# Kernel optimization log

Measured on AMD Instinct MI355X. Metric: run time of the kernel, lower is better.

Reference implementation:

```python
import jax, jax.numpy as jnp
import numpy as np

B, N, IN_F = 4, 2048, 256
H, HEAD_DIM = 8, 32  # out_features=256, concat=True -> head_dim=32
ALPHA = 0.2
MASK_VAL = -9e15


def setup_inputs() -> dict:
    key = jax.random.key(0)
    k1, k2, k3, k4 = jax.random.split(key, 4)
    x = jax.random.normal(k1, (B, N, IN_F), dtype=jnp.float32)
    adj = jax.random.randint(k2, (B, N, N), 0, 2, dtype=jnp.int32)
    # xavier_uniform for W [H, in, head_dim]: gain=1, fan_in=in, fan_out=head_dim
    limW = float(np.sqrt(6.0 / (IN_F + HEAD_DIM)))
    W = jax.random.uniform(k3, (H, IN_F, HEAD_DIM), dtype=jnp.float32, minval=-limW, maxval=limW)
    # xavier_uniform for a [H, 2*head_dim]: fan_in=2*head_dim, fan_out=H (2D tensor)
    lima = float(np.sqrt(6.0 / (H + 2 * HEAD_DIM)))
    a = jax.random.uniform(k4, (H, 2 * HEAD_DIM), dtype=jnp.float32, minval=-lima, maxval=lima)
    return {"x": x, "adj": adj, "W": W, "a": a}


def reference(x, adj, W, a):
    # x: [B, N, F], adj: [B, N, N], W: [H, F, D], a: [H, 2D]
    D = W.shape[-1]
    Wh = jnp.einsum('bnf,hfd->bhnd', x, W)                     # [B,H,N,D]
    a_src, a_dst = a[:, :D], a[:, D:]
    # additive score e_ij = a_src . Wh_i + a_dst . Wh_j (equivalent to concat+matmul)
    e_i = jnp.einsum('bhnd,hd->bhn', Wh, a_src)                # [B,H,N]
    e_j = jnp.einsum('bhnd,hd->bhn', Wh, a_dst)                # [B,H,N]
    scores = e_i[:, :, :, None] + e_j[:, :, None, :]           # [B,H,N,N]
    scores = jnp.where(scores > 0, scores, ALPHA * scores)     # LeakyReLU
    scores = jnp.where(adj[:, None, :, :] == 0, MASK_VAL, scores)
    probs = jax.nn.softmax(scores, axis=-1)                    # [B,H,N,N]
    h = jnp.einsum('bhij,bhjd->bhid', probs, Wh)               # [B,H,N,D]
    b, n = x.shape[0], x.shape[1]
    return h.transpose(0, 2, 1, 3).reshape(b, n, h.shape[1] * D)  # concat heads
```

## Files before the change

### kernel.cpp

```cpp
#include <hip/hip_runtime.h>

#define BB 4
#define NN 2048
#define INF 256
#define HH 8
#define DD 32
#define LOG2E 1.4426950408889634f

typedef __attribute__((ext_vector_type(8))) short short8;
typedef __attribute__((ext_vector_type(4))) float f32x4;

__device__ __forceinline__ unsigned short bf16_rhu(float v) {
    return (unsigned short)((__float_as_uint(v) + 0x8000u) >> 16);
}

__global__ __launch_bounds__(256) void we_kernel(
    const float* __restrict__ W, const float* __restrict__ a, float* __restrict__ we_g)
{
    const int k = blockIdx.x;
    const int h = k & 7, sel = k >> 3;
    const int f = threadIdx.x;
    const float* wr = W + ((size_t)h * INF + f) * DD;
    const float* av = a + h * 2 * DD + sel * DD;
    float acc = 0.f;
    #pragma unroll
    for (int d = 0; d < DD; ++d) acc += wr[d] * av[d];
    we_g[k * INF + f] = acc * LOG2E;
}

__global__ __launch_bounds__(256) void prep_kernel(
    const float* __restrict__ x, const float* __restrict__ W,
    const float* __restrict__ we_g, unsigned short* __restrict__ xbf,
    unsigned short* __restrict__ wT, float* __restrict__ esrc, float* __restrict__ edst)
{
    __shared__ __align__(16) float weld[16 * 256];
    const int t = threadIdx.x;
    #pragma unroll
    for (int i = 0; i < 4; ++i)
        *(f32x4*)&weld[i * 1024 + t * 4] = *(const f32x4*)&we_g[i * 1024 + t * 4];
    if (blockIdx.x < 32) {
        #pragma unroll
        for (int r2 = 0; r2 < 8; ++r2) {
            int row = blockIdx.x * 8 + r2;
            int h = row >> 5, d = row & 31;
            wT[row * INF + t] = bf16_rhu(W[((size_t)h * INF + t) * DD + d]);
        }
    }
    __syncthreads();
    const int wv = t >> 6, l = t & 63;
    const int rr = l >> 4, c = l & 15;
    const int gr = blockIdx.x * 16 + wv * 4 + rr;
    const int b = gr >> 11, n = gr & 2047;
    const float* xr = x + (size_t)gr * INF + c * 16;
    f32x4 xx[4];
    #pragma unroll
    for (int i = 0; i < 4; ++i) xx[i] = *(const f32x4*)&xr[i * 4];
    unsigned pk[8];
    #pragma unroll
    for (int i = 0; i < 8; ++i) {
        unsigned lo = __float_as_uint(xx[i >> 1][(i & 1) * 2]) + 0x8000u;
        unsigned hi = __float_as_uint(xx[i >> 1][(i & 1) * 2 + 1]) + 0x8000u;
        pk[i] = __builtin_amdgcn_perm(hi, lo, 0x07060302u);
    }
    *(uint4*)&xbf[(size_t)gr * INF + c * 16] = *(uint4*)&pk[0];
    *(uint4*)&xbf[(size_t)gr * INF + c * 16 + 8] = *(uint4*)&pk[4];
    #pragma unroll
    for (int k = 0; k < 16; ++k) {
        const float* wk = &weld[k * 256 + c * 16];
        float s = 0.f;
        #pragma unroll
        for (int i = 0; i < 4; ++i) {
            f32x4 w4 = *(const f32x4*)&wk[i * 4];
            s += xx[i][0]*w4[0] + xx[i][1]*w4[1] + xx[i][2]*w4[2] + xx[i][3]*w4[3];
        }
        s += __shfl_xor(s, 1, 64);
        s += __shfl_xor(s, 2, 64);
        s += __shfl_xor(s, 4, 64);
        s += __shfl_xor(s, 8, 64);
        if (c == k) {
            if (k < 8) esrc[(b * 8 + k) * NN + n] = s;
            else       edst[(b * 8 + (k - 8)) * NN + n] = s;
        }
    }
}

__global__ __launch_bounds__(512) void wh_kernel(
    const unsigned short* __restrict__ xbf, const unsigned short* __restrict__ wT,
    unsigned short* __restrict__ whT2)
{
    __shared__ __align__(16) unsigned short xb[128 * 264];
    __shared__ __align__(16) unsigned short wb[64 * 264];
    const int t = threadIdx.x;
    const int hp = blockIdx.x & 3, ntile = (blockIdx.x >> 2) & 15, b = blockIdx.x >> 6;
    const int n0 = ntile * 128;
    #pragma unroll
    for (int p = 0; p < 8; ++p) {
        int flat = p * 4096 + t * 8;
        int row = flat >> 8, col = flat & 255;
        *(short8*)&xb[row * 264 + col] =
            *(const short8*)&xbf[((size_t)b * NN + n0 + row) * INF + col];
    }
    #pragma unroll
    for (int p = 0; p < 4; ++p) {
        int flat = p * 4096 + t * 8;
        int cc = flat >> 8, f = flat & 255;
        *(short8*)&wb[cc * 264 + f] = *(const short8*)&wT[(hp * 64 + cc) * INF + f];
    }
    __syncthreads();
    const int w = t >> 6, l = t & 63;
    const int wm = w & 3, wn = w >> 2;
    const int ml = l & 15, q = l >> 4;
    f32x4 acc[2][2] = {};
    const unsigned short* a0p = &xb[(wm * 32 + ml) * 264 + q * 8];
    const unsigned short* a1p = &xb[(wm * 32 + 16 + ml) * 264 + q * 8];
    const unsigned short* b0p = &wb[(wn * 32 + ml) * 264 + q * 8];
    const unsigned short* b1p = &wb[(wn * 32 + 16 + ml) * 264 + q * 8];
    #pragma unroll
    for (int k0 = 0; k0 < INF; k0 += 32) {
        short8 A0 = *(const short8*)&a0p[k0];
        short8 A1 = *(const short8*)&a1p[k0];
        short8 B0 = *(const short8*)&b0p[k0];
        short8 B1 = *(const short8*)&b1p[k0];
        acc[0][0] = __builtin_amdgcn_mfma_f32_16x16x32_bf16(A0, B0, acc[0][0], 0, 0, 0);
        acc[0][1] = __builtin_amdgcn_mfma_f32_16x16x32_bf16(A0, B1, acc[0][1], 0, 0, 0);
        acc[1][0] = __builtin_amdgcn_mfma_f32_16x16x32_bf16(A1, B0, acc[1][0], 0, 0, 0);
        acc[1][1] = __builtin_amdgcn_mfma_f32_16x16x32_bf16(A1, B1, acc[1][1], 0, 0, 0);
    }
    __syncthreads();
    unsigned short* ldsC = xb;
    #pragma unroll
    for (int mt = 0; mt < 2; ++mt)
        #pragma unroll
        for (int nt = 0; nt < 2; ++nt)
            #pragma unroll
            for (int r = 0; r < 4; ++r) {
                int ct = wn * 32 + nt * 16 + ml;
                int rt = wm * 32 + mt * 16 + q * 4 + r;
                ldsC[ct * 136 + rt] = bf16_rhu(acc[mt][nt][r]);
            }
    __syncthreads();
    #pragma unroll
    for (int p = 0; p < 2; ++p) {
        int g = p * 512 + t;
        int d = g & 31, jo = (g >> 5) & 15, h2 = g >> 9;
        short8 vv = *(const short8*)&ldsC[(h2 * 32 + d) * 136 + jo * 8];
        int bh = b * 8 + hp * 2 + h2;
        *(short8*)&whT2[(((size_t)bh * 256 + ntile * 16 + jo) * 32 + d) * 8] = vv;
    }
}

__global__ __launch_bounds__(1024, 4) void attn_kernel(
    const int* __restrict__ adj, const unsigned short* __restrict__ whT2,
    const float* __restrict__ esrc, const float* __restrict__ edst,
    float* __restrict__ out)
{
    __shared__ __align__(16) unsigned bits[2][2][32][4];
    __shared__ __align__(16) float cmb[8][64][24];
    const int t = threadIdx.x, v = t >> 6, l = t & 63;
    const int h = v & 7, js = v >> 3;
    const int ml = l & 15, q = l >> 4;
    const int it = blockIdx.x & 63, b = blockIdx.x >> 6;
    const int i0 = it * 32;
    const int bh = b * HH + h;
    const float ei0 = esrc[bh * NN + i0 + ml];
    const float ei1 = esrc[bh * NN + i0 + 16 + ml];
    const float* ejp = edst + bh * NN + js * 1024;
    const unsigned short* whb = whT2 + ((size_t)bh * 256 + js * 128) * 256;

    auto stage = [&](int c2, int buf) {
        #pragma unroll
        for (int u = 0; u < 4; ++u) {
            int uid = v * 4 + u;
            int row = uid & 31, half = uid >> 5;
            const int* g = adj + ((size_t)(b * NN + i0 + row)) * NN + half * 1024 + c2 * 128 + l;
            int a0 = g[0], a1 = g[64];
            unsigned long long m0 = __ballot(a0 != 0);
            unsigned long long m1 = __ballot(a1 != 0);
            if (l == 0) {
                uint4 pv = make_uint4((unsigned)m0, (unsigned)(m0 >> 32),
                                      (unsigned)m1, (unsigned)(m1 >> 32));
                *(uint4*)&bits[buf][half][row][0] = pv;
            }
        }
    };

    const short8 ones = {0x3F80, 0x3F80, 0x3F80, 0x3F80, 0x3F80, 0x3F80, 0x3F80, 0x3F80};
    f32x4 acc00 = {}, acc01 = {}, acc10 = {}, acc11 = {}, accD0 = {}, accD1 = {};

    stage(0, 0);
    for (int c = 0; c < 8; ++c) {
        __syncthreads();
        if (c < 7) stage(c + 1, (c + 1) & 1);
        const int buf = c & 1;
        unsigned w0a[4], w1a[4];
        *(uint4*)w0a = *(const uint4*)&bits[buf][js][ml][0];
        *(uint4*)w1a = *(const uint4*)&bits[buf][js][16 + ml][0];
        const float* ejc = ejp + c * 128;
        #pragma unroll
        for (int k = 0; k < 4; ++k) {
            const int jb = k * 32 + q * 8;
            f32x4 ejA = *(const f32x4*)&ejc[jb];
            f32x4 ejB = *(const f32x4*)&ejc[jb + 4];
            const unsigned short* wp = whb + (size_t)(c * 16 + k * 4 + q) * 256;
            short8 B0 = *(const short8*)&wp[ml * 8];
            short8 B1 = *(const short8*)&wp[(16 + ml) * 8];
            unsigned st0 = w0a[k] >> (q * 8);
            unsigned st1 = w1a[k] >> (q * 8);
            union { unsigned u[4]; short8 s; } f0, f1;
            #pragma unroll
            for (int pp = 0; pp < 4; ++pp) {
                float eA = (pp < 2) ? ejA[pp * 2] : ejB[pp * 2 - 4];
                float eB = (pp < 2) ? ejA[pp * 2 + 1] : ejB[pp * 2 - 3];
                unsigned mA0 = (unsigned)__builtin_amdgcn_sbfe(st0, 2 * pp, 1);
                unsigned mB0 = (unsigned)__builtin_amdgcn_sbfe(st0, 2 * pp + 1, 1);
                unsigned mA1 = (unsigned)__builtin_amdgcn_sbfe(st1, 2 * pp, 1);
                unsigned mB1 = (unsigned)__builtin_amdgcn_sbfe(st1, 2 * pp + 1, 1);
                float z; unsigned pa, pb;
                z = ei0 + eA; z = fmaxf(z, 0.2f * z);
                pa = (__float_as_uint(__builtin_amdgcn_exp2f(z)) + 0x8000u) & mA0;
                z = ei0 + eB; z = fmaxf(z, 0.2f * z);
                pb = (__float_as_uint(__builtin_amdgcn_exp2f(z)) + 0x8000u) & mB0;
                f0.u[pp] = __builtin_amdgcn_perm(pb, pa, 0x07060302u);
                z = ei1 + eA; z = fmaxf(z, 0.2f * z);
                pa = (__float_as_uint(__builtin_amdgcn_exp2f(z)) + 0x8000u) & mA1;
                z = ei1 + eB; z = fmaxf(z, 0.2f * z);
                pb = (__float_as_uint(__builtin_amdgcn_exp2f(z)) + 0x8000u) & mB1;
                f1.u[pp] = __builtin_amdgcn_perm(pb, pa, 0x07060302u);
            }
            acc00 = __builtin_amdgcn_mfma_f32_16x16x32_bf16(f0.s, B0, acc00, 0, 0, 0);
            acc01 = __builtin_amdgcn_mfma_f32_16x16x32_bf16(f0.s, B1, acc01, 0, 0, 0);
            accD0 = __builtin_amdgcn_mfma_f32_16x16x32_bf16(f0.s, ones, accD0, 0, 0, 0);
            acc10 = __builtin_amdgcn_mfma_f32_16x16x32_bf16(f1.s, B0, acc10, 0, 0, 0);
            acc11 = __builtin_amdgcn_mfma_f32_16x16x32_bf16(f1.s, B1, acc11, 0, 0, 0);
            accD1 = __builtin_amdgcn_mfma_f32_16x16x32_bf16(f1.s, ones, accD1, 0, 0, 0);
        }
    }

    float* myc = &cmb[h][l][0];
    if (js == 1) {
        *(f32x4*)&myc[0]  = acc00; *(f32x4*)&myc[4]  = acc01;
        *(f32x4*)&myc[8]  = acc10; *(f32x4*)&myc[12] = acc11;
        *(f32x4*)&myc[16] = accD0; *(f32x4*)&myc[20] = accD1;
    }
    __syncthreads();
    if (js == 0) {
        f32x4 o00 = *(const f32x4*)&myc[0],  o01 = *(const f32x4*)&myc[4];
        f32x4 o10 = *(const f32x4*)&myc[8],  o11 = *(const f32x4*)&myc[12];
        f32x4 oD0 = *(const f32x4*)&myc[16], oD1 = *(const f32x4*)&myc[20];
        #pragma unroll
        for (int r = 0; r < 4; ++r) {
            int ir0 = i0 + q * 4 + r;
            int ir1 = i0 + 16 + q * 4 + r;
            float inv0 = 1.0f / (accD0[r] + oD0[r]);
            float inv1 = 1.0f / (accD1[r] + oD1[r]);
            size_t ba0 = ((size_t)(b * NN + ir0)) * (HH * DD) + h * DD;
            size_t ba1 = ((size_t)(b * NN + ir1)) * (HH * DD) + h * DD;
            out[ba0 + ml]      = (acc00[r] + o00[r]) * inv0;
            out[ba0 + 16 + ml] = (acc01[r] + o01[r]) * inv0;
            out[ba1 + ml]      = (acc10[r] + o10[r]) * inv1;
            out[ba1 + 16 + ml] = (acc11[r] + o11[r]) * inv1;
        }
    }
}

extern "C" void kernel_launch(void* const* d_in, const int* in_sizes, int n_in,
                              void* d_out, int out_size, void* d_ws, size_t ws_size,
                              hipStream_t stream) {
    (void)in_sizes; (void)n_in; (void)out_size; (void)ws_size;
    const float* x   = (const float*)d_in[0];
    const int*   adj = (const int*)d_in[1];
    const float* W   = (const float*)d_in[2];
    const float* a   = (const float*)d_in[3];
    float* out = (float*)d_out;

    char* ws = (char*)d_ws;
    unsigned short* whT2 = (unsigned short*)ws;
    unsigned short* xbf  = (unsigned short*)(ws + (4u << 20));
    unsigned short* wT   = (unsigned short*)(ws + (8u << 20));
    float* esrc = (float*)(ws + (8u << 20) + (128u << 10));
    float* edst = esrc + BB * HH * NN;
    float* we_g = edst + BB * HH * NN;

    we_kernel<<<dim3(16), dim3(256), 0, stream>>>(W, a, we_g);
    prep_kernel<<<dim3(512), dim3(256), 0, stream>>>(x, W, we_g, xbf, wT, esrc, edst);
    wh_kernel<<<dim3(256), dim3(512), 0, stream>>>(xbf, wT, whT2);
    attn_kernel<<<dim3(256), dim3(1024), 0, stream>>>(adj, whT2, esrc, edst, out);
}
```

Baseline: 161.5 us.

## Factor exp of LeakyReLU score into precomputed per-node exponentials and halve row tile

```diff
diff --git a/kernel.cpp b/kernel.cpp
--- a/kernel.cpp
+++ b/kernel.cpp
@@ -31,7 +31,8 @@
 __global__ __launch_bounds__(256) void prep_kernel(
     const float* __restrict__ x, const float* __restrict__ W,
     const float* __restrict__ we_g, unsigned short* __restrict__ xbf,
-    unsigned short* __restrict__ wT, float* __restrict__ esrc, float* __restrict__ edst)
+    unsigned short* __restrict__ wT, float* __restrict__ esrc,
+    float* __restrict__ ejE, float* __restrict__ ejE5)
 {
     __shared__ __align__(16) float weld[16 * 256];
     const int t = threadIdx.x;
@@ -78,8 +79,12 @@
         s += __shfl_xor(s, 4, 64);
         s += __shfl_xor(s, 8, 64);
         if (c == k) {
-            if (k < 8) esrc[(b * 8 + k) * NN + n] = s;
-            else       edst[(b * 8 + (k - 8)) * NN + n] = s;
+            if (k < 8) {
+                esrc[(b * 8 + k) * NN + n] = s;
+            } else {
+                ejE [(b * 8 + (k - 8)) * NN + n] = __builtin_amdgcn_exp2f(s);
+                ejE5[(b * 8 + (k - 8)) * NN + n] = __builtin_amdgcn_exp2f(0.2f * s);
+            }
         }
     }
 }
@@ -149,116 +154,106 @@
     }
 }
 
-__global__ __launch_bounds__(1024, 4) void attn_kernel(
+__global__ __launch_bounds__(1024, 8) void attn_kernel(
     const int* __restrict__ adj, const unsigned short* __restrict__ whT2,
-    const float* __restrict__ esrc, const float* __restrict__ edst,
-    float* __restrict__ out)
-{
-    __shared__ __align__(16) unsigned bits[2][2][32][4];
-    __shared__ __align__(16) float cmb[8][64][24];
+    const float* __restrict__ esrc, const float* __restrict__ ejE,
+    const float* __restrict__ ejE5, float* __restrict__ out)
+{
+    __shared__ __align__(16) unsigned bits[2][2][16][4];
+    __shared__ __align__(16) float cmb[8][64][12];
     const int t = threadIdx.x, v = t >> 6, l = t & 63;
     const int h = v & 7, js = v >> 3;
     const int ml = l & 15, q = l >> 4;
-    const int it = blockIdx.x & 63, b = blockIdx.x >> 6;
-    const int i0 = it * 32;
+    const int it = blockIdx.x & 127, b = blockIdx.x >> 7;
+    const int i0 = it * 16;
     const int bh = b * HH + h;
-    const float ei0 = esrc[bh * NN + i0 + ml];
-    const float ei1 = esrc[bh * NN + i0 + 16 + ml];
-    const float* ejp = edst + bh * NN + js * 1024;
+
+    const float ei  = esrc[bh * NN + i0 + ml];
+    const float Ei  = __builtin_amdgcn_exp2f(ei);
+    const float Ei5 = __builtin_amdgcn_exp2f(0.2f * ei);
+    const float Ti  = __builtin_amdgcn_exp2f(-ei);
+
+    const float* EjP  = ejE  + bh * NN + js * 1024;
+    const float* FjP  = ejE5 + bh * NN + js * 1024;
     const unsigned short* whb = whT2 + ((size_t)bh * 256 + js * 128) * 256;
 
     auto stage = [&](int c2, int buf) {
         #pragma unroll
         for (int u = 0; u < 4; ++u) {
-            int uid = v * 4 + u;
-            int row = uid & 31, half = uid >> 5;
-            const int* g = adj + ((size_t)(b * NN + i0 + row)) * NN + half * 1024 + c2 * 128 + l;
-            int a0 = g[0], a1 = g[64];
+            int uid = h * 4 + u;
+            int row = uid & 15, half = uid >> 4;
+            const int* g = adj + ((size_t)(b * NN + i0 + row)) * NN
+                               + js * 1024 + c2 * 128 + half * 64 + l;
+            int a0 = g[0];
             unsigned long long m0 = __ballot(a0 != 0);
-            unsigned long long m1 = __ballot(a1 != 0);
-            if (l == 0) {
-                uint4 pv = make_uint4((unsigned)m0, (unsigned)(m0 >> 32),
-                                      (unsigned)m1, (unsigned)(m1 >> 32));
-                *(uint4*)&bits[buf][half][row][0] = pv;
-            }
+            if (l == 0)
+                *(uint2*)&bits[js][buf][row][half * 2] =
+                    make_uint2((unsigned)m0, (unsigned)(m0 >> 32));
         }
     };
 
     const short8 ones = {0x3F80, 0x3F80, 0x3F80, 0x3F80, 0x3F80, 0x3F80, 0x3F80, 0x3F80};
-    f32x4 acc00 = {}, acc01 = {}, acc10 = {}, acc11 = {}, accD0 = {}, accD1 = {};
+    f32x4 acc0 = {}, acc1 = {}, accD = {};
 
     stage(0, 0);
     for (int c = 0; c < 8; ++c) {
         __syncthreads();
         if (c < 7) stage(c + 1, (c + 1) & 1);
         const int buf = c & 1;
-        unsigned w0a[4], w1a[4];
-        *(uint4*)w0a = *(const uint4*)&bits[buf][js][ml][0];
-        *(uint4*)w1a = *(const uint4*)&bits[buf][js][16 + ml][0];
-        const float* ejc = ejp + c * 128;
+        unsigned wa[4];
+        *(uint4*)wa = *(const uint4*)&bits[js][buf][ml][0];
+        const float* ejc = EjP + c * 128;
+        const float* fjc = FjP + c * 128;
         #pragma unroll
         for (int k = 0; k < 4; ++k) {
             const int jb = k * 32 + q * 8;
-            f32x4 ejA = *(const f32x4*)&ejc[jb];
-            f32x4 ejB = *(const f32x4*)&ejc[jb + 4];
+            f32x4 EA = *(const f32x4*)&ejc[jb];
+            f32x4 EB = *(const f32x4*)&ejc[jb + 4];
+            f32x4 FA = *(const f32x4*)&fjc[jb];
+            f32x4 FB = *(const f32x4*)&fjc[jb + 4];
             const unsigned short* wp = whb + (size_t)(c * 16 + k * 4 + q) * 256;
             short8 B0 = *(const short8*)&wp[ml * 8];
             short8 B1 = *(const short8*)&wp[(16 + ml) * 8];
-            unsigned st0 = w0a[k] >> (q * 8);
-            unsigned st1 = w1a[k] >> (q * 8);
-            union { unsigned u[4]; short8 s; } f0, f1;
+            unsigned st = wa[k] >> (q * 8);
+            union { unsigned u[4]; short8 s; } f0;
             #pragma unroll
             for (int pp = 0; pp < 4; ++pp) {
-                float eA = (pp < 2) ? ejA[pp * 2] : ejB[pp * 2 - 4];
-                float eB = (pp < 2) ? ejA[pp * 2 + 1] : ejB[pp * 2 - 3];
-                unsigned mA0 = (unsigned)__builtin_amdgcn_sbfe(st0, 2 * pp, 1);
-                unsigned mB0 = (unsigned)__builtin_amdgcn_sbfe(st0, 2 * pp + 1, 1);
-                unsigned mA1 = (unsigned)__builtin_amdgcn_sbfe(st1, 2 * pp, 1);
-                unsigned mB1 = (unsigned)__builtin_amdgcn_sbfe(st1, 2 * pp + 1, 1);
-                float z; unsigned pa, pb;
-                z = ei0 + eA; z = fmaxf(z, 0.2f * z);
-                pa = (__float_as_uint(__builtin_amdgcn_exp2f(z)) + 0x8000u) & mA0;
-                z = ei0 + eB; z = fmaxf(z, 0.2f * z);
-                pb = (__float_as_uint(__builtin_amdgcn_exp2f(z)) + 0x8000u) & mB0;
-                f0.u[pp] = __builtin_amdgcn_perm(pb, pa, 0x07060302u);
-                z = ei1 + eA; z = fmaxf(z, 0.2f * z);
-                pa = (__float_as_uint(__builtin_amdgcn_exp2f(z)) + 0x8000u) & mA1;
-                z = ei1 + eB; z = fmaxf(z, 0.2f * z);
-                pb = (__float_as_uint(__builtin_amdgcn_exp2f(z)) + 0x8000u) & mB1;
-                f1.u[pp] = __builtin_amdgcn_perm(pb, pa, 0x07060302u);
+                float eA = (pp < 2) ? EA[2 * pp]     : EB[2 * pp - 4];
+                float eB = (pp < 2) ? EA[2 * pp + 1] : EB[2 * pp - 3];
+                float fA = (pp < 2) ? FA[2 * pp]     : FB[2 * pp - 4];
+                float fB = (pp < 2) ? FA[2 * pp + 1] : FB[2 * pp - 3];
+                float pA = (eA > Ti) ? eA * Ei : fA * Ei5;
+                float pB = (eB > Ti) ? eB * Ei : fB * Ei5;
+                unsigned mA = (unsigned)__builtin_amdgcn_sbfe(st, 2 * pp, 1);
+                unsigned mB = (unsigned)__builtin_amdgcn_sbfe(st, 2 * pp + 1, 1);
+                unsigned ra = (__float_as_uint(pA) + 0x8000u) & mA;
+                unsigned rb = (__float_as_uint(pB) + 0x8000u) & mB;
+                f0.u[pp] = __builtin_amdgcn_perm(rb, ra, 0x07060302u);
             }
-            acc00 = __builtin_amdgcn_mfma_f32_16x16x32_bf16(f0.s, B0, acc00, 0, 0, 0);
-            acc01 = __builtin_amdgcn_mfma_f32_16x16x32_bf16(f0.s, B1, acc01, 0, 0, 0);
-            accD0 = __builtin_amdgcn_mfma_f32_16x16x32_bf16(f0.s, ones, accD0, 0, 0, 0);
-            acc10 = __builtin_amdgcn_mfma_f32_16x16x32_bf16(f1.s, B0, acc10, 0, 0, 0);
-            acc11 = __builtin_amdgcn_mfma_f32_16x16x32_bf16(f1.s, B1, acc11, 0, 0, 0);
-            accD1 = __builtin_amdgcn_mfma_f32_16x16x32_bf16(f1.s, ones, accD1, 0, 0, 0);
+            acc0 = __builtin_amdgcn_mfma_f32_16x16x32_bf16(f0.s, B0, acc0, 0, 0, 0);
+            acc1 = __builtin_amdgcn_mfma_f32_16x16x32_bf16(f0.s, B1, acc1, 0, 0, 0);
+            accD = __builtin_amdgcn_mfma_f32_16x16x32_bf16(f0.s, ones, accD, 0, 0, 0);
         }
     }
 
     float* myc = &cmb[h][l][0];
     if (js == 1) {
-        *(f32x4*)&myc[0]  = acc00; *(f32x4*)&myc[4]  = acc01;
-        *(f32x4*)&myc[8]  = acc10; *(f32x4*)&myc[12] = acc11;
-        *(f32x4*)&myc[16] = accD0; *(f32x4*)&myc[20] = accD1;
+        *(f32x4*)&myc[0] = acc0;
+        *(f32x4*)&myc[4] = acc1;
+        *(f32x4*)&myc[8] = accD;
     }
     __syncthreads();
     if (js == 0) {
-        f32x4 o00 = *(const f32x4*)&myc[0],  o01 = *(const f32x4*)&myc[4];
-        f32x4 o10 = *(const f32x4*)&myc[8],  o11 = *(const f32x4*)&myc[12];
-        f32x4 oD0 = *(const f32x4*)&myc[16], oD1 = *(const f32x4*)&myc[20];
+        f32x4 o0 = *(const f32x4*)&myc[0];
+        f32x4 o1 = *(const f32x4*)&myc[4];
+        f32x4 oD = *(const f32x4*)&myc[8];
         #pragma unroll
         for (int r = 0; r < 4; ++r) {
-            int ir0 = i0 + q * 4 + r;
-            int ir1 = i0 + 16 + q * 4 + r;
-            float inv0 = 1.0f / (accD0[r] + oD0[r]);
-            float inv1 = 1.0f / (accD1[r] + oD1[r]);
-            size_t ba0 = ((size_t)(b * NN + ir0)) * (HH * DD) + h * DD;
-            size_t ba1 = ((size_t)(b * NN + ir1)) * (HH * DD) + h * DD;
-            out[ba0 + ml]      = (acc00[r] + o00[r]) * inv0;
-            out[ba0 + 16 + ml] = (acc01[r] + o01[r]) * inv0;
-            out[ba1 + ml]      = (acc10[r] + o10[r]) * inv1;
-            out[ba1 + 16 + ml] = (acc11[r] + o11[r]) * inv1;
+            int ir = i0 + q * 4 + r;
+            float inv = 1.0f / (accD[r] + oD[r]);
+            size_t ba = ((size_t)(b * NN + ir)) * (HH * DD) + h * DD;
+            out[ba + ml]      = (acc0[r] + o0[r]) * inv;
+            out[ba + 16 + ml] = (acc1[r] + o1[r]) * inv;
         }
     }
 }
@@ -278,11 +273,12 @@
     unsigned short* xbf  = (unsigned short*)(ws + (4u << 20));
     unsigned short* wT   = (unsigned short*)(ws + (8u << 20));
     float* esrc = (float*)(ws + (8u << 20) + (128u << 10));
-    float* edst = esrc + BB * HH * NN;
-    float* we_g = edst + BB * HH * NN;
+    float* ejE  = esrc + BB * HH * NN;
+    float* ejE5 = ejE + BB * HH * NN;
+    float* we_g = ejE5 + BB * HH * NN;
 
     we_kernel<<<dim3(16), dim3(256), 0, stream>>>(W, a, we_g);
-    prep_kernel<<<dim3(512), dim3(256), 0, stream>>>(x, W, we_g, xbf, wT, esrc, edst);
+    prep_kernel<<<dim3(512), dim3(256), 0, stream>>>(x, W, we_g, xbf, wT, esrc, ejE, ejE5);
     wh_kernel<<<dim3(256), dim3(512), 0, stream>>>(xbf, wT, whT2);
-    attn_kernel<<<dim3(256), dim3(1024), 0, stream>>>(adj, whT2, esrc, edst, out);
-}
+    attn_kernel<<<dim3(512), dim3(1024), 0, stream>>>(adj, whT2, esrc, ejE, ejE5, out);
+}
```

Measured after the change: 171.8 us. +6.4%, slower.

## Factor exp of LeakyReLU scores into precomputed per-node exponentials, drop extra kernels

Applied to the files above, without the earlier changes.

```diff
diff --git a/kernel.cpp b/kernel.cpp
--- a/kernel.cpp
+++ b/kernel.cpp
@@ -10,40 +10,36 @@
 typedef __attribute__((ext_vector_type(8))) short short8;
 typedef __attribute__((ext_vector_type(4))) float f32x4;
 
+__device__ __forceinline__ unsigned short bf16_rne(float v) {
+    unsigned b = __float_as_uint(v);
+    return (unsigned short)((b + 0x7fffu + ((b >> 16) & 1u)) >> 16);
+}
 __device__ __forceinline__ unsigned short bf16_rhu(float v) {
     return (unsigned short)((__float_as_uint(v) + 0x8000u) >> 16);
 }
 
-__global__ __launch_bounds__(256) void we_kernel(
-    const float* __restrict__ W, const float* __restrict__ a, float* __restrict__ we_g)
-{
-    const int k = blockIdx.x;
-    const int h = k & 7, sel = k >> 3;
-    const int f = threadIdx.x;
-    const float* wr = W + ((size_t)h * INF + f) * DD;
-    const float* av = a + h * 2 * DD + sel * DD;
-    float acc = 0.f;
-    #pragma unroll
-    for (int d = 0; d < DD; ++d) acc += wr[d] * av[d];
-    we_g[k * INF + f] = acc * LOG2E;
-}
-
 __global__ __launch_bounds__(256) void prep_kernel(
     const float* __restrict__ x, const float* __restrict__ W,
-    const float* __restrict__ we_g, unsigned short* __restrict__ xbf,
-    unsigned short* __restrict__ wT, float* __restrict__ esrc, float* __restrict__ edst)
+    const float* __restrict__ a, unsigned short* __restrict__ wT,
+    float* __restrict__ esrc, unsigned* __restrict__ ejP)
 {
     __shared__ __align__(16) float weld[16 * 256];
     const int t = threadIdx.x;
-    #pragma unroll
-    for (int i = 0; i < 4; ++i)
-        *(f32x4*)&weld[i * 1024 + t * 4] = *(const f32x4*)&we_g[i * 1024 + t * 4];
+    for (int k = 0; k < 16; ++k) {
+        int h = k & 7, sel = k >> 3;
+        const float* wr = W + ((size_t)(h * INF + t)) * DD;
+        const float* av = a + h * 2 * DD + sel * DD;
+        float acc = 0.f;
+        #pragma unroll
+        for (int d = 0; d < DD; ++d) acc += wr[d] * av[d];
+        weld[k * 256 + t] = acc * LOG2E;
+    }
     if (blockIdx.x < 32) {
         #pragma unroll
         for (int r2 = 0; r2 < 8; ++r2) {
             int row = blockIdx.x * 8 + r2;
             int h = row >> 5, d = row & 31;
-            wT[row * INF + t] = bf16_rhu(W[((size_t)h * INF + t) * DD + d]);
+            wT[row * INF + t] = bf16_rhu(W[((size_t)(h * INF + t)) * DD + d]);
         }
     }
     __syncthreads();
@@ -55,15 +51,6 @@
     f32x4 xx[4];
     #pragma unroll
     for (int i = 0; i < 4; ++i) xx[i] = *(const f32x4*)&xr[i * 4];
-    unsigned pk[8];
-    #pragma unroll
-    for (int i = 0; i < 8; ++i) {
-        unsigned lo = __float_as_uint(xx[i >> 1][(i & 1) * 2]) + 0x8000u;
-        unsigned hi = __float_as_uint(xx[i >> 1][(i & 1) * 2 + 1]) + 0x8000u;
-        pk[i] = __builtin_amdgcn_perm(hi, lo, 0x07060302u);
-    }
-    *(uint4*)&xbf[(size_t)gr * INF + c * 16] = *(uint4*)&pk[0];
-    *(uint4*)&xbf[(size_t)gr * INF + c * 16 + 8] = *(uint4*)&pk[4];
     #pragma unroll
     for (int k = 0; k < 16; ++k) {
         const float* wk = &weld[k * 256 + c * 16];
@@ -78,14 +65,20 @@
         s += __shfl_xor(s, 4, 64);
         s += __shfl_xor(s, 8, 64);
         if (c == k) {
-            if (k < 8) esrc[(b * 8 + k) * NN + n] = s;
-            else       edst[(b * 8 + (k - 8)) * NN + n] = s;
+            if (k < 8) {
+                esrc[(b * 8 + k) * NN + n] = s;
+            } else {
+                float Ej  = __builtin_amdgcn_exp2f(s);
+                float Ej5 = __builtin_amdgcn_exp2f(0.2f * s);
+                ejP[(b * 8 + (k - 8)) * NN + n] =
+                    ((unsigned)bf16_rne(Ej) << 16) | (unsigned)bf16_rne(Ej5);
+            }
         }
     }
 }
 
 __global__ __launch_bounds__(512) void wh_kernel(
-    const unsigned short* __restrict__ xbf, const unsigned short* __restrict__ wT,
+    const float* __restrict__ x, const unsigned short* __restrict__ wT,
     unsigned short* __restrict__ whT2)
 {
     __shared__ __align__(16) unsigned short xb[128 * 264];
@@ -94,11 +87,18 @@
     const int hp = blockIdx.x & 3, ntile = (blockIdx.x >> 2) & 15, b = blockIdx.x >> 6;
     const int n0 = ntile * 128;
     #pragma unroll
-    for (int p = 0; p < 8; ++p) {
-        int flat = p * 4096 + t * 8;
+    for (int p = 0; p < 16; ++p) {
+        int flat = p * 2048 + t * 4;
         int row = flat >> 8, col = flat & 255;
-        *(short8*)&xb[row * 264 + col] =
-            *(const short8*)&xbf[((size_t)b * NN + n0 + row) * INF + col];
+        f32x4 g = *(const f32x4*)&x[((size_t)(b * NN + n0 + row)) * INF + col];
+        unsigned a0 = __float_as_uint(g[0]) + 0x8000u;
+        unsigned a1 = __float_as_uint(g[1]) + 0x8000u;
+        unsigned a2 = __float_as_uint(g[2]) + 0x8000u;
+        unsigned a3 = __float_as_uint(g[3]) + 0x8000u;
+        uint2 pk;
+        pk.x = __builtin_amdgcn_perm(a1, a0, 0x07060302u);
+        pk.y = __builtin_amdgcn_perm(a3, a2, 0x07060302u);
+        *(uint2*)&xb[row * 264 + col] = pk;
     }
     #pragma unroll
     for (int p = 0; p < 4; ++p) {
@@ -151,7 +151,7 @@
 
 __global__ __launch_bounds__(1024, 4) void attn_kernel(
     const int* __restrict__ adj, const unsigned short* __restrict__ whT2,
-    const float* __restrict__ esrc, const float* __restrict__ edst,
+    const float* __restrict__ esrc, const unsigned* __restrict__ ejP,
     float* __restrict__ out)
 {
     __shared__ __align__(16) unsigned bits[2][2][32][4];
@@ -162,9 +162,15 @@
     const int it = blockIdx.x & 63, b = blockIdx.x >> 6;
     const int i0 = it * 32;
     const int bh = b * HH + h;
+
     const float ei0 = esrc[bh * NN + i0 + ml];
     const float ei1 = esrc[bh * NN + i0 + 16 + ml];
-    const float* ejp = edst + bh * NN + js * 1024;
+    const float Ei0  = __builtin_amdgcn_exp2f(ei0);
+    const float Ei05 = __builtin_amdgcn_exp2f(0.2f * ei0);
+    const float Ei1  = __builtin_amdgcn_exp2f(ei1);
+    const float Ei15 = __builtin_amdgcn_exp2f(0.2f * ei1);
+
+    const unsigned* epP = ejP + bh * NN + js * 1024;
     const unsigned short* whb = whT2 + ((size_t)bh * 256 + js * 128) * 256;
 
     auto stage = [&](int c2, int buf) {
@@ -172,7 +178,8 @@
         for (int u = 0; u < 4; ++u) {
             int uid = v * 4 + u;
             int row = uid & 31, half = uid >> 5;
-            const int* g = adj + ((size_t)(b * NN + i0 + row)) * NN + half * 1024 + c2 * 128 + l;
+            const int* g = adj + ((size_t)(b * NN + i0 + row)) * NN
+                               + half * 1024 + c2 * 128 + l;
             int a0 = g[0], a1 = g[64];
             unsigned long long m0 = __ballot(a0 != 0);
             unsigned long long m1 = __ballot(a1 != 0);
@@ -195,37 +202,42 @@
         unsigned w0a[4], w1a[4];
         *(uint4*)w0a = *(const uint4*)&bits[buf][js][ml][0];
         *(uint4*)w1a = *(const uint4*)&bits[buf][js][16 + ml][0];
-        const float* ejc = ejp + c * 128;
+        const unsigned* epc = epP + c * 128;
         #pragma unroll
         for (int k = 0; k < 4; ++k) {
             const int jb = k * 32 + q * 8;
-            f32x4 ejA = *(const f32x4*)&ejc[jb];
-            f32x4 ejB = *(const f32x4*)&ejc[jb + 4];
+            uint4 epA = *(const uint4*)&epc[jb];
+            uint4 epB = *(const uint4*)&epc[jb + 4];
             const unsigned short* wp = whb + (size_t)(c * 16 + k * 4 + q) * 256;
             short8 B0 = *(const short8*)&wp[ml * 8];
             short8 B1 = *(const short8*)&wp[(16 + ml) * 8];
             unsigned st0 = w0a[k] >> (q * 8);
             unsigned st1 = w1a[k] >> (q * 8);
             union { unsigned u[4]; short8 s; } f0, f1;
+            const unsigned* ea = &epA.x;
+            const unsigned* eb = &epB.x;
             #pragma unroll
             for (int pp = 0; pp < 4; ++pp) {
-                float eA = (pp < 2) ? ejA[pp * 2] : ejB[pp * 2 - 4];
-                float eB = (pp < 2) ? ejA[pp * 2 + 1] : ejB[pp * 2 - 3];
+                unsigned pkA = (pp < 2) ? ea[2 * pp]     : eb[2 * pp - 4];
+                unsigned pkB = (pp < 2) ? ea[2 * pp + 1] : eb[2 * pp - 3];
+                float EjA = __uint_as_float(pkA & 0xffff0000u);
+                float FjA = __uint_as_float(pkA << 16);
+                float EjB = __uint_as_float(pkB & 0xffff0000u);
+                float FjB = __uint_as_float(pkB << 16);
                 unsigned mA0 = (unsigned)__builtin_amdgcn_sbfe(st0, 2 * pp, 1);
                 unsigned mB0 = (unsigned)__builtin_amdgcn_sbfe(st0, 2 * pp + 1, 1);
                 unsigned mA1 = (unsigned)__builtin_amdgcn_sbfe(st1, 2 * pp, 1);
                 unsigned mB1 = (unsigned)__builtin_amdgcn_sbfe(st1, 2 * pp + 1, 1);
-                float z; unsigned pa, pb;
-                z = ei0 + eA; z = fmaxf(z, 0.2f * z);
-                pa = (__float_as_uint(__builtin_amdgcn_exp2f(z)) + 0x8000u) & mA0;
-                z = ei0 + eB; z = fmaxf(z, 0.2f * z);
-                pb = (__float_as_uint(__builtin_amdgcn_exp2f(z)) + 0x8000u) & mB0;
-                f0.u[pp] = __builtin_amdgcn_perm(pb, pa, 0x07060302u);
-                z = ei1 + eA; z = fmaxf(z, 0.2f * z);
-                pa = (__float_as_uint(__builtin_amdgcn_exp2f(z)) + 0x8000u) & mA1;
-                z = ei1 + eB; z = fmaxf(z, 0.2f * z);
-                pb = (__float_as_uint(__builtin_amdgcn_exp2f(z)) + 0x8000u) & mB1;
-                f1.u[pp] = __builtin_amdgcn_perm(pb, pa, 0x07060302u);
+                float pA0 = fmaxf(EjA * Ei0, FjA * Ei05);
+                float pB0 = fmaxf(EjB * Ei0, FjB * Ei05);
+                float pA1 = fmaxf(EjA * Ei1, FjA * Ei15);
+                float pB1 = fmaxf(EjB * Ei1, FjB * Ei15);
+                f0.u[pp] = __builtin_amdgcn_perm(__float_as_uint(pB0) & mB0,
+                                                 __float_as_uint(pA0) & mA0,
+                                                 0x07060302u);
+                f1.u[pp] = __builtin_amdgcn_perm(__float_as_uint(pB1) & mB1,
+                                                 __float_as_uint(pA1) & mA1,
+                                                 0x07060302u);
             }
             acc00 = __builtin_amdgcn_mfma_f32_16x16x32_bf16(f0.s, B0, acc00, 0, 0, 0);
             acc01 = __builtin_amdgcn_mfma_f32_16x16x32_bf16(f0.s, B1, acc01, 0, 0, 0);
@@ -275,14 +287,11 @@
 
     char* ws = (char*)d_ws;
     unsigned short* whT2 = (unsigned short*)ws;
-    unsigned short* xbf  = (unsigned short*)(ws + (4u << 20));
-    unsigned short* wT   = (unsigned short*)(ws + (8u << 20));
-    float* esrc = (float*)(ws + (8u << 20) + (128u << 10));
-    float* edst = esrc + BB * HH * NN;
-    float* we_g = edst + BB * HH * NN;
-
-    we_kernel<<<dim3(16), dim3(256), 0, stream>>>(W, a, we_g);
-    prep_kernel<<<dim3(512), dim3(256), 0, stream>>>(x, W, we_g, xbf, wT, esrc, edst);
-    wh_kernel<<<dim3(256), dim3(512), 0, stream>>>(xbf, wT, whT2);
-    attn_kernel<<<dim3(256), dim3(1024), 0, stream>>>(adj, whT2, esrc, edst, out);
-}
+    unsigned short* wT   = (unsigned short*)(ws + (4u << 20));
+    float*    esrc = (float*)(ws + (4u << 20) + (128u << 10));
+    unsigned* ejP  = (unsigned*)(esrc + BB * HH * NN);
+
+    prep_kernel<<<dim3(512), dim3(256), 0, stream>>>(x, W, a, wT, esrc, ejP);
+    wh_kernel<<<dim3(256), dim3(512), 0, stream>>>(x, wT, whT2);
+    attn_kernel<<<dim3(256), dim3(1024), 0, stream>>>(adj, whT2, esrc, ejP, out);
+}
```

Result: slower. 180.7 us (+11.9%).
